# Optimization experiments

Hardware: AMD Instinct MI355X
Metric: run time of the kernel (lower is better)

The kernel has to match this reference:

```python
import jax, jax.numpy as jnp
import numpy as np

LP, LQ, B, IN, HID = 256, 256, 32, 512, 512
H = 2 * HID          # internal hidden size (hidden_size * 2)
IN2 = 2 * IN         # Up/Uq feature dim after self-concat
IN4 = 4 * IN


def setup_inputs() -> dict:
    key = jax.random.key(0)
    ks = jax.random.split(key, 12)
    def w(k, shape, fan):
        return (jax.random.normal(k, shape, jnp.float32) / np.float32(np.sqrt(fan)))
    return {
        "up": jax.random.normal(ks[0], (LP, B, IN), jnp.float32),
        "uq": jax.random.normal(ks[1], (LQ, B, IN), jnp.float32),
        "v0": jax.random.normal(ks[2], (B, H), jnp.float32),    # torch.randn v
        "Vvec": jax.random.normal(ks[3], (B, H), jnp.float32),  # torch.randn V (squeezed)
        "Wp": w(ks[4], (H, IN2), IN2),
        "Wq": w(ks[5], (H, IN2), IN2),
        "Wv": w(ks[6], (H, H), H),
        "Wg": w(ks[7], (IN4, IN4), IN4),
        "W_ih": w(ks[8], (3 * H, IN2), IN2),
        "W_hh": w(ks[9], (3 * H, H), H),
        "b_ih": w(ks[10], (3 * H,), H),
        "b_hh": w(ks[11], (3 * H,), H),
    }


def reference(up, uq, v0, Vvec, Wp, Wq, Wv, Wg, W_ih, W_hh, b_ih, b_hh):
    in2 = 2 * up.shape[2]
    # mixer indices are arange -> Up/Uq are just feature self-concats
    Up = jnp.concatenate([up, up], axis=2)   # [lp, B, in2]
    Uq = jnp.concatenate([uq, uq], axis=2)   # [lq, B, in2]
    # hoist loop-invariant projections (original recomputes Wq(Uq) each step)
    WUp = jnp.einsum('pbi,hi->pbh', Up, Wp)  # [lp, B, H]
    WUq = jnp.einsum('qbi,hi->qbh', Uq, Wq)  # [lq, B, H]

    def gru_cell(x, h):
        gi = x @ W_ih.T + b_ih
        gh = h @ W_hh.T + b_hh
        i_r, i_z, i_n = jnp.split(gi, 3, axis=1)
        h_r, h_z, h_n = jnp.split(gh, 3, axis=1)
        r = jax.nn.sigmoid(i_r + h_r)
        z = jax.nn.sigmoid(i_z + h_z)
        n = jnp.tanh(i_n + r * h_n)
        return (1.0 - z) * n + z * h

    def step(v, xs):
        up_i, wup_i = xs                                   # [B,in2], [B,H]
        x = jnp.tanh(wup_i[None] + WUq + (v @ Wv.T)[None])  # [lq, B, H]
        s = jnp.einsum('qbh,bh->bq', x, Vvec)               # [B, lq]
        a = jax.nn.softmax(s, axis=1)
        c = jnp.einsum('bq,qbd->bd', a, Uq)                 # [B, in2]
        r = jnp.concatenate([up_i, c], axis=1)              # [B, in4]
        g = jax.nn.sigmoid(r @ Wg.T)
        c_ = (g * r)[:, in2:]                               # gated context half
        v_new = gru_cell(c_, v)
        return v_new, v_new

    _, vs = jax.lax.scan(step, v0, (Up, WUp))   # vs: [lp, B, H]
    # dropout in eval mode = identity
    return vs
```

## Files before the change

### kernel.cpp

```cpp
#include <hip/hip_runtime.h>


#define NB 32
#define H 1024
#define H3 3072
#define LQn 256
#define LPn 256

__device__ __forceinline__ float fsig(float x) { return 1.0f / (1.0f + __expf(-x)); }
__device__ __forceinline__ float ftanh(float x) { return 1.0f - 2.0f / (1.0f + __expf(2.0f * x)); }

__global__ __launch_bounds__(256) void k_init(
    const float* __restrict__ v0, const float* __restrict__ Wp,
    const float* __restrict__ Wg, float* __restrict__ vbuf0,
    float* __restrict__ Wpf, float* __restrict__ Wg2f) {
  int i = blockIdx.x * 256 + threadIdx.x;
  if (i < NB * H) vbuf0[i] = v0[i];
  if (i < 1024 * 512) {
    int n = i >> 9, k = i & 511;
    Wpf[i] = Wp[(size_t)n * 1024 + k] + Wp[(size_t)n * 1024 + k + 512];
  }
  if (i < 1024 * 1024) {
    int j = i >> 10, kk = i & 1023;
    const float* wr = Wg + (size_t)(1024 + j) * 2048;
    Wg2f[i] = (kk < 512) ? (wr[kk] + wr[kk + 512]) : (wr[kk + 512] + wr[kk + 1024]);
  }
}

__global__ __launch_bounds__(256) void k_wuq(
    const float* __restrict__ A, const float* __restrict__ Wq, float* __restrict__ C) {
  __shared__ float As[16][65];
  __shared__ float Bs[16][65];
  int bm = blockIdx.x * 64, bn = blockIdx.y * 64;
  int t = threadIdx.x;
  int tx = t & 15, ty = t >> 4;
  float acc[4][4] = {};
  for (int k0 = 0; k0 < 512; k0 += 16) {
#pragma unroll
    for (int l = 0; l < 4; ++l) {
      int idx = t + l * 256;
      int row = idx >> 4, kk = idx & 15;
      As[kk][row] = A[(size_t)(bm + row) * 512 + k0 + kk];
      Bs[kk][row] = Wq[(size_t)(bn + row) * 1024 + k0 + kk] +
                    Wq[(size_t)(bn + row) * 1024 + k0 + kk + 512];
    }
    __syncthreads();
#pragma unroll
    for (int kk = 0; kk < 16; ++kk) {
      float a0[4], b0[4];
#pragma unroll
      for (int i = 0; i < 4; ++i) a0[i] = As[kk][ty * 4 + i];
#pragma unroll
      for (int j = 0; j < 4; ++j) b0[j] = Bs[kk][tx * 4 + j];
#pragma unroll
      for (int i = 0; i < 4; ++i)
#pragma unroll
        for (int j = 0; j < 4; ++j) acc[i][j] += a0[i] * b0[j];
    }
    __syncthreads();
  }
#pragma unroll
  for (int i = 0; i < 4; ++i)
#pragma unroll
    for (int j = 0; j < 4; ++j)
      C[(size_t)(bm + ty * 4 + i) * 1024 + bn + tx * 4 + j] = acc[i][j];
}

__global__ __launch_bounds__(256, 1) void k_A(
    const float* __restrict__ gi, const float* __restrict__ gh_old,
    const float* __restrict__ v_old, const float* __restrict__ up,
    const float* __restrict__ Wv, const float* __restrict__ W_hh,
    const float* __restrict__ b_hh, const float* __restrict__ Wpf,
    float* __restrict__ v_new_g, float* __restrict__ out,
    float* __restrict__ t_out, float* __restrict__ gh_new, int p) {
  int s = blockIdx.x & 63, bg = blockIdx.x >> 6;
  int b0 = bg * 8;
  int tid = threadIdx.x, lane = tid & 63, wave = tid >> 6;
  __shared__ float vnew[8][H];
  __shared__ float upb[8][512];

  if (p == 0) {
    for (int bb = 0; bb < 8; ++bb)
#pragma unroll
      for (int ii = 0; ii < 4; ++ii) {
        int h = tid + ii * 256;
        vnew[bb][h] = v_old[(size_t)(b0 + bb) * H + h];
      }
  } else {
    for (int bb = 0; bb < 8; ++bb) {
      int b = b0 + bb;
      const float* gib = gi + (size_t)b * H3;
      const float* ghb = gh_old + (size_t)b * H3;
#pragma unroll
      for (int ii = 0; ii < 4; ++ii) {
        int h = tid + ii * 256;
        float rg = fsig(gib[h] + ghb[h]);
        float z = fsig(gib[H + h] + ghb[H + h]);
        float nn = ftanh(gib[2 * H + h] + rg * ghb[2 * H + h]);
        float vo = v_old[(size_t)b * H + h];
        float vn = (1.0f - z) * nn + z * vo;
        vnew[bb][h] = vn;
        if (s == 0) {
          v_new_g[(size_t)b * H + h] = vn;
          out[((size_t)(p - 1) * NB + b) * H + h] = vn;
        }
      }
    }
  }
  bool is_t = (s < 16);
  if (is_t) {
    for (int idx = tid; idx < 8 * 512; idx += 256) {
      int bb = idx >> 9, k = idx & 511;
      upb[bb][k] = up[((size_t)p * NB + (b0 + bb)) * 512 + k];
    }
  }
  __syncthreads();

  float vreg[8][16];
#pragma unroll
  for (int bb = 0; bb < 8; ++bb)
#pragma unroll
    for (int i = 0; i < 16; ++i) vreg[bb][i] = vnew[bb][lane + i * 64];

  int n0 = s * 64 + wave * 16;
  for (int rr = 0; rr < 16; ++rr) {
    int n = n0 + rr;
    float acc[8];
#pragma unroll
    for (int bb = 0; bb < 8; ++bb) acc[bb] = 0.0f;
    if (is_t) {
      const float* wr = Wv + (size_t)n * H;
#pragma unroll
      for (int i = 0; i < 16; ++i) {
        float w = wr[lane + i * 64];
#pragma unroll
        for (int bb = 0; bb < 8; ++bb) acc[bb] = fmaf(w, vreg[bb][i], acc[bb]);
      }
      const float* wp = Wpf + (size_t)n * 512;
#pragma unroll
      for (int i = 0; i < 8; ++i) {
        float w = wp[lane + i * 64];
#pragma unroll
        for (int bb = 0; bb < 8; ++bb) acc[bb] = fmaf(w, upb[bb][lane + i * 64], acc[bb]);
      }
#pragma unroll
      for (int bb = 0; bb < 8; ++bb) {
        float a = acc[bb];
#pragma unroll
        for (int o = 32; o >= 1; o >>= 1) a += __shfl_xor(a, o, 64);
        if (lane == 0) t_out[(size_t)(b0 + bb) * H + n] = a;
      }
    } else {
      int m = n - H;
      const float* wr = W_hh + (size_t)m * H;
#pragma unroll
      for (int i = 0; i < 16; ++i) {
        float w = wr[lane + i * 64];
#pragma unroll
        for (int bb = 0; bb < 8; ++bb) acc[bb] = fmaf(w, vreg[bb][i], acc[bb]);
      }
      float bias = b_hh[m];
#pragma unroll
      for (int bb = 0; bb < 8; ++bb) {
        float a = acc[bb];
#pragma unroll
        for (int o = 32; o >= 1; o >>= 1) a += __shfl_xor(a, o, 64);
        if (lane == 0) gh_new[(size_t)(b0 + bb) * H3 + m] = a + bias;
      }
    }
  }
}

__global__ __launch_bounds__(64) void k_B(
    const float* __restrict__ t_in, const float* __restrict__ WUq,
    const float* __restrict__ Vvec, float* __restrict__ s_out) {
  int q = blockIdx.x >> 5, b = blockIdx.x & 31;
  int lane = threadIdx.x;
  const float* wq = WUq + ((size_t)q * NB + b) * H;
  const float* tb = t_in + (size_t)b * H;
  const float* vv = Vvec + (size_t)b * H;
  float a = 0.0f;
#pragma unroll
  for (int i = 0; i < 16; ++i) {
    int h = lane + i * 64;
    a += ftanh(tb[h] + wq[h]) * vv[h];
  }
#pragma unroll
  for (int o = 32; o >= 1; o >>= 1) a += __shfl_xor(a, o, 64);
  if (lane == 0) s_out[b * LQn + q] = a;
}

__global__ __launch_bounds__(256) void k_C(
    const float* __restrict__ s_in, const float* __restrict__ uq,
    const float* __restrict__ up, float* __restrict__ rhalf, int p) {
  int b = blockIdx.x;
  int tid = threadIdx.x, lane = tid & 63, wave = tid >> 6;
  __shared__ float a_s[256];
  __shared__ float red[4];
  float sv = s_in[b * LQn + tid];
  float m = sv;
#pragma unroll
  for (int o = 32; o >= 1; o >>= 1) m = fmaxf(m, __shfl_xor(m, o, 64));
  if (lane == 0) red[wave] = m;
  __syncthreads();
  float bm = fmaxf(fmaxf(red[0], red[1]), fmaxf(red[2], red[3]));
  __syncthreads();
  float e = __expf(sv - bm);
  float se = e;
#pragma unroll
  for (int o = 32; o >= 1; o >>= 1) se += __shfl_xor(se, o, 64);
  if (lane == 0) red[wave] = se;
  __syncthreads();
  float tot = red[0] + red[1] + red[2] + red[3];
  a_s[tid] = e / tot;
  __syncthreads();
  rhalf[(size_t)b * 1024 + tid] = up[((size_t)p * NB + b) * 512 + tid];
  rhalf[(size_t)b * 1024 + tid + 256] = up[((size_t)p * NB + b) * 512 + tid + 256];
  float acc0 = 0.0f, acc1 = 0.0f;
  for (int q = 0; q < LQn; ++q) {
    float a = a_s[q];
    const float* uqr = uq + ((size_t)q * NB + b) * 512;
    acc0 += a * uqr[tid];
    acc1 += a * uqr[tid + 256];
  }
  rhalf[(size_t)b * 1024 + 512 + tid] = acc0;
  rhalf[(size_t)b * 1024 + 512 + tid + 256] = acc1;
}

__global__ __launch_bounds__(256, 1) void k_D(
    const float* __restrict__ rhalf, const float* __restrict__ Wg2f,
    float* __restrict__ c_g) {
  int s = blockIdx.x & 63, bg = blockIdx.x >> 6, b0 = bg * 8;
  int tid = threadIdx.x, lane = tid & 63, wave = tid >> 6;
  float rreg[8][16];
#pragma unroll
  for (int bb = 0; bb < 8; ++bb)
#pragma unroll
    for (int i = 0; i < 16; ++i)
      rreg[bb][i] = rhalf[(size_t)(b0 + bb) * 1024 + lane + i * 64];
  int j0 = s * 16 + wave * 4;
  for (int rr = 0; rr < 4; ++rr) {
    int j = j0 + rr;
    const float* wr = Wg2f + (size_t)j * 1024;
    float acc[8];
#pragma unroll
    for (int bb = 0; bb < 8; ++bb) acc[bb] = 0.0f;
#pragma unroll
    for (int i = 0; i < 16; ++i) {
      float w = wr[lane + i * 64];
#pragma unroll
      for (int bb = 0; bb < 8; ++bb) acc[bb] = fmaf(w, rreg[bb][i], acc[bb]);
    }
#pragma unroll
    for (int bb = 0; bb < 8; ++bb) {
      float a = acc[bb];
#pragma unroll
      for (int o = 32; o >= 1; o >>= 1) a += __shfl_xor(a, o, 64);
      if (lane == 0) {
        float cv = rhalf[(size_t)(b0 + bb) * 1024 + 512 + (j & 511)];
        c_g[(size_t)(b0 + bb) * 1024 + j] = fsig(a) * cv;
      }
    }
  }
}

__global__ __launch_bounds__(256, 1) void k_E(
    const float* __restrict__ c_g, const float* __restrict__ W_ih,
    const float* __restrict__ b_ih, float* __restrict__ gi) {
  int s = blockIdx.x & 63, bg = blockIdx.x >> 6, b0 = bg * 8;
  int tid = threadIdx.x, lane = tid & 63, wave = tid >> 6;
  float creg[8][16];
#pragma unroll
  for (int bb = 0; bb < 8; ++bb)
#pragma unroll
    for (int i = 0; i < 16; ++i)
      creg[bb][i] = c_g[(size_t)(b0 + bb) * 1024 + lane + i * 64];
  int r0 = s * 48 + wave * 12;
  for (int rr = 0; rr < 12; ++rr) {
    int r = r0 + rr;
    const float* wr = W_ih + (size_t)r * 1024;
    float acc[8];
#pragma unroll
    for (int bb = 0; bb < 8; ++bb) acc[bb] = 0.0f;
#pragma unroll
    for (int i = 0; i < 16; ++i) {
      float w = wr[lane + i * 64];
#pragma unroll
      for (int bb = 0; bb < 8; ++bb) acc[bb] = fmaf(w, creg[bb][i], acc[bb]);
    }
    float bias = b_ih[r];
#pragma unroll
    for (int bb = 0; bb < 8; ++bb) {
      float a = acc[bb];
#pragma unroll
      for (int o = 32; o >= 1; o >>= 1) a += __shfl_xor(a, o, 64);
      if (lane == 0) gi[(size_t)(b0 + bb) * H3 + r] = a + bias;
    }
  }
}

__global__ __launch_bounds__(256) void k_fin(
    const float* __restrict__ gi, const float* __restrict__ gh_old,
    const float* __restrict__ v_old, float* __restrict__ out) {
  int i = blockIdx.x * 256 + threadIdx.x;
  int b = i >> 10, h = i & 1023;
  const float* gib = gi + (size_t)b * H3;
  const float* ghb = gh_old + (size_t)b * H3;
  float rg = fsig(gib[h] + ghb[h]);
  float z = fsig(gib[H + h] + ghb[H + h]);
  float nn = ftanh(gib[2 * H + h] + rg * ghb[2 * H + h]);
  float vn = (1.0f - z) * nn + z * v_old[i];
  out[(size_t)255 * NB * H + i] = vn;
}

extern "C" void kernel_launch(void* const* d_in, const int* in_sizes, int n_in,
                              void* d_out, int out_size, void* d_ws, size_t ws_size,
                              hipStream_t stream) {
  const float* up = (const float*)d_in[0];
  const float* uq = (const float*)d_in[1];
  const float* v0 = (const float*)d_in[2];
  const float* Vvec = (const float*)d_in[3];
  const float* Wp = (const float*)d_in[4];
  const float* Wq = (const float*)d_in[5];
  const float* Wv = (const float*)d_in[6];
  const float* Wg = (const float*)d_in[7];
  const float* W_ih = (const float*)d_in[8];
  const float* W_hh = (const float*)d_in[9];
  const float* b_ih = (const float*)d_in[10];
  const float* b_hh = (const float*)d_in[11];
  float* out = (float*)d_out;
  float* ws = (float*)d_ws;

  float* vbuf0 = ws;
  float* vbuf1 = ws + 32768;
  float* tbuf  = ws + 65536;
  float* gh0   = ws + 98304;
  float* gh1   = ws + 196608;
  float* sbuf  = ws + 294912;
  float* rhalf = ws + 303104;
  float* cbuf  = ws + 335872;
  float* gibuf = ws + 368640;
  float* Wpf   = ws + 466944;
  float* Wg2f  = ws + 991232;
  float* WUq   = ws + 2039808;

  k_init<<<4096, 256, 0, stream>>>(v0, Wp, Wg, vbuf0, Wpf, Wg2f);
  k_wuq<<<dim3(128, 16), 256, 0, stream>>>(uq, Wq, WUq);

  for (int p = 0; p < 256; ++p) {
    float* ghn = (p & 1) ? gh1 : gh0;
    float* gho = (p & 1) ? gh0 : gh1;
    float* vn = (p & 1) ? vbuf1 : vbuf0;
    float* vo = (p & 1) ? vbuf0 : vbuf1;
    if (p == 0) { vo = vbuf0; vn = vbuf1; }
    k_A<<<256, 256, 0, stream>>>(gibuf, gho, vo, up, Wv, W_hh, b_hh, Wpf,
                                 vn, out, tbuf, ghn, p);
    k_B<<<8192, 64, 0, stream>>>(tbuf, WUq, Vvec, sbuf);
    k_C<<<32, 256, 0, stream>>>(sbuf, uq, up, rhalf, p);
    k_D<<<256, 256, 0, stream>>>(rhalf, Wg2f, cbuf);
    k_E<<<256, 256, 0, stream>>>(cbuf, W_ih, b_ih, gibuf);
  }
  k_fin<<<128, 256, 0, stream>>>(gibuf, gh1, vbuf1, out);
}
```

Baseline: 29.62 ms.

## Replace per-step kernel launches with persistent kernel using grid barriers

Merges the five per-timestep kernels and the final kernel into one persistent kernel of 256 blocks × 512 threads. The kernel loops over all 256 steps and separates phases with a software global barrier built on atomics. The GRU update moves into the W_ih phase through shared memory, and the attention-context phase is split across 256 blocks instead of 32. This removes about 1280 launch overheads and gaps. It depends on all 256 blocks being co-resident for the spin barrier, and each barrier adds atomic latency.

```diff
diff --git a/kernel.cpp b/kernel.cpp
--- a/kernel.cpp
+++ b/kernel.cpp
@@ -2,20 +2,41 @@
 
 
 #define NB 32
-#define H 1024
-#define H3 3072
-#define LQn 256
-#define LPn 256
 
 __device__ __forceinline__ float fsig(float x) { return 1.0f / (1.0f + __expf(-x)); }
 __device__ __forceinline__ float ftanh(float x) { return 1.0f - 2.0f / (1.0f + __expf(2.0f * x)); }
 
+__device__ __forceinline__ float wred(float a) {
+#pragma unroll
+  for (int o = 32; o >= 1; o >>= 1) a += __shfl_xor(a, o, 64);
+  return a;
+}
+
+__device__ __forceinline__ void gbar(int* cnt, int* gen) {
+  __syncthreads();
+  if (threadIdx.x == 0) {
+    __threadfence();
+    int g = __hip_atomic_load(gen, __ATOMIC_RELAXED, __HIP_MEMORY_SCOPE_AGENT);
+    int a = __hip_atomic_fetch_add(cnt, 1, __ATOMIC_ACQ_REL, __HIP_MEMORY_SCOPE_AGENT);
+    if (a == 255) {
+      __hip_atomic_store(cnt, 0, __ATOMIC_RELAXED, __HIP_MEMORY_SCOPE_AGENT);
+      __hip_atomic_store(gen, g + 1, __ATOMIC_RELEASE, __HIP_MEMORY_SCOPE_AGENT);
+    } else {
+      while (__hip_atomic_load(gen, __ATOMIC_ACQUIRE, __HIP_MEMORY_SCOPE_AGENT) == g)
+        __builtin_amdgcn_s_sleep(2);
+    }
+    __threadfence();
+  }
+  __syncthreads();
+}
+
 __global__ __launch_bounds__(256) void k_init(
     const float* __restrict__ v0, const float* __restrict__ Wp,
-    const float* __restrict__ Wg, float* __restrict__ vbuf0,
-    float* __restrict__ Wpf, float* __restrict__ Wg2f) {
+    const float* __restrict__ Wg, float* __restrict__ wsbase,
+    float* __restrict__ vbuf, float* __restrict__ Wpf, float* __restrict__ Wg2f) {
   int i = blockIdx.x * 256 + threadIdx.x;
-  if (i < NB * H) vbuf0[i] = v0[i];
+  if (i < 64) ((int*)wsbase)[i] = 0;
+  if (i < NB * 1024) vbuf[i] = v0[i];
   if (i < 1024 * 512) {
     int n = i >> 9, k = i & 511;
     Wpf[i] = Wp[(size_t)n * 1024 + k] + Wp[(size_t)n * 1024 + k + 512];
@@ -66,251 +87,241 @@
       C[(size_t)(bm + ty * 4 + i) * 1024 + bn + tx * 4 + j] = acc[i][j];
 }
 
-__global__ __launch_bounds__(256, 1) void k_A(
-    const float* __restrict__ gi, const float* __restrict__ gh_old,
-    const float* __restrict__ v_old, const float* __restrict__ up,
-    const float* __restrict__ Wv, const float* __restrict__ W_hh,
-    const float* __restrict__ b_hh, const float* __restrict__ Wpf,
-    float* __restrict__ v_new_g, float* __restrict__ out,
-    float* __restrict__ t_out, float* __restrict__ gh_new, int p) {
-  int s = blockIdx.x & 63, bg = blockIdx.x >> 6;
-  int b0 = bg * 8;
+__global__ __launch_bounds__(512, 2) void k_loop(
+    const float* __restrict__ up, const float* __restrict__ uq,
+    const float* __restrict__ Vvec, const float* __restrict__ Wv,
+    const float* __restrict__ W_hh, const float* __restrict__ b_hh,
+    const float* __restrict__ W_ih, const float* __restrict__ b_ih,
+    float* __restrict__ out, float* __restrict__ ws) {
+  int* cnt = (int*)ws;
+  int* gen = ((int*)ws) + 32;
+  float* vbuf  = ws + 64;
+  float* tbuf  = ws + 32832;
+  float* ghbuf = ws + 65600;
+  float* sbuf  = ws + 163904;
+  float* chalf = ws + 172096;
+  float* cbuf  = ws + 188480;
+  float* Wpf   = ws + 221248;
+  float* Wg2f  = ws + 745536;
+  float* WUq   = ws + 1794112;
+
+  int bid = blockIdx.x;
   int tid = threadIdx.x, lane = tid & 63, wave = tid >> 6;
-  __shared__ float vnew[8][H];
-  __shared__ float upb[8][512];
-
-  if (p == 0) {
-    for (int bb = 0; bb < 8; ++bb)
-#pragma unroll
-      for (int ii = 0; ii < 4; ++ii) {
-        int h = tid + ii * 256;
-        vnew[bb][h] = v_old[(size_t)(b0 + bb) * H + h];
-      }
-  } else {
-    for (int bb = 0; bb < 8; ++bb) {
-      int b = b0 + bb;
-      const float* gib = gi + (size_t)b * H3;
-      const float* ghb = gh_old + (size_t)b * H3;
-#pragma unroll
-      for (int ii = 0; ii < 4; ++ii) {
-        int h = tid + ii * 256;
-        float rg = fsig(gib[h] + ghb[h]);
-        float z = fsig(gib[H + h] + ghb[H + h]);
-        float nn = ftanh(gib[2 * H + h] + rg * ghb[2 * H + h]);
-        float vo = v_old[(size_t)b * H + h];
+
+  __shared__ float smem[4096];
+
+  int s = bid & 63, bg = bid >> 6, b0 = bg * 8;
+  bool is_t = (s < 16);
+  int b3 = bid >> 3, i0 = (bid & 7) * 64;
+
+  for (int p = 0; p < 256; ++p) {
+    {
+      float vreg[8][16];
+#pragma unroll
+      for (int bb = 0; bb < 8; ++bb)
+#pragma unroll
+        for (int i = 0; i < 16; ++i)
+          vreg[bb][i] = vbuf[(size_t)(b0 + bb) * 1024 + lane + i * 64];
+      if (is_t) {
+        for (int idx = tid; idx < 4096; idx += 512) {
+          int bb = idx >> 9, k = idx & 511;
+          smem[idx] = up[((size_t)p * NB + b0 + bb) * 512 + k];
+        }
+      }
+      __syncthreads();
+      int n0 = s * 64 + wave * 8;
+      for (int rr = 0; rr < 8; ++rr) {
+        int n = n0 + rr;
+        float acc[8];
+#pragma unroll
+        for (int bb = 0; bb < 8; ++bb) acc[bb] = 0.0f;
+        if (is_t) {
+          const float* wr = Wv + (size_t)n * 1024;
+#pragma unroll
+          for (int i = 0; i < 16; ++i) {
+            float w = wr[lane + i * 64];
+#pragma unroll
+            for (int bb = 0; bb < 8; ++bb) acc[bb] = fmaf(w, vreg[bb][i], acc[bb]);
+          }
+          const float* wp = Wpf + (size_t)n * 512;
+#pragma unroll
+          for (int i = 0; i < 8; ++i) {
+            float w = wp[lane + i * 64];
+#pragma unroll
+            for (int bb = 0; bb < 8; ++bb)
+              acc[bb] = fmaf(w, smem[bb * 512 + lane + i * 64], acc[bb]);
+          }
+#pragma unroll
+          for (int bb = 0; bb < 8; ++bb) {
+            float a = wred(acc[bb]);
+            if (lane == 0) tbuf[(size_t)(b0 + bb) * 1024 + n] = a;
+          }
+        } else {
+          int m = n - 1024;
+          const float* wr = W_hh + (size_t)m * 1024;
+#pragma unroll
+          for (int i = 0; i < 16; ++i) {
+            float w = wr[lane + i * 64];
+#pragma unroll
+            for (int bb = 0; bb < 8; ++bb) acc[bb] = fmaf(w, vreg[bb][i], acc[bb]);
+          }
+          float bias = b_hh[m];
+#pragma unroll
+          for (int bb = 0; bb < 8; ++bb) {
+            float a = wred(acc[bb]);
+            if (lane == 0) ghbuf[(size_t)(b0 + bb) * 3072 + m] = a + bias;
+          }
+        }
+      }
+    }
+    gbar(cnt, gen);
+
+    {
+      int gw = bid * 8 + wave;
+      int b = gw & 31, q0 = (gw >> 5) * 4;
+      float treg[16], vvreg[16];
+#pragma unroll
+      for (int i = 0; i < 16; ++i) {
+        treg[i]  = tbuf[(size_t)b * 1024 + lane + i * 64];
+        vvreg[i] = Vvec[(size_t)b * 1024 + lane + i * 64];
+      }
+      for (int qq = 0; qq < 4; ++qq) {
+        int q = q0 + qq;
+        const float* wu = WUq + ((size_t)q * NB + b) * 1024;
+        float a = 0.0f;
+#pragma unroll
+        for (int i = 0; i < 16; ++i)
+          a += ftanh(treg[i] + wu[lane + i * 64]) * vvreg[i];
+        a = wred(a);
+        if (lane == 0) sbuf[b * 256 + q] = a;
+      }
+    }
+    gbar(cnt, gen);
+
+    {
+      float* a_s  = smem;
+      float* red  = smem + 256;
+      float* part = smem + 512;
+      int b = b3;
+      float sv = -1e30f;
+      if (tid < 256) sv = sbuf[b * 256 + tid];
+      float m = sv;
+#pragma unroll
+      for (int o = 32; o >= 1; o >>= 1) m = fmaxf(m, __shfl_xor(m, o, 64));
+      if (lane == 0 && wave < 4) red[wave] = m;
+      __syncthreads();
+      float bm = fmaxf(fmaxf(red[0], red[1]), fmaxf(red[2], red[3]));
+      __syncthreads();
+      float e = 0.0f;
+      if (tid < 256) e = __expf(sv - bm);
+      float se = e;
+#pragma unroll
+      for (int o = 32; o >= 1; o >>= 1) se += __shfl_xor(se, o, 64);
+      if (lane == 0 && wave < 4) red[wave] = se;
+      __syncthreads();
+      float tot = red[0] + red[1] + red[2] + red[3];
+      if (tid < 256) a_s[tid] = e / tot;
+      __syncthreads();
+      float acc = 0.0f;
+      for (int qq = 0; qq < 32; ++qq) {
+        int q = wave * 32 + qq;
+        acc += a_s[q] * uq[((size_t)q * NB + b) * 512 + i0 + lane];
+      }
+      part[wave * 64 + lane] = acc;
+      __syncthreads();
+      if (tid < 64) {
+        float c = 0.0f;
+#pragma unroll
+        for (int w = 0; w < 8; ++w) c += part[w * 64 + tid];
+        chalf[(size_t)b * 512 + i0 + tid] = c;
+      }
+    }
+    gbar(cnt, gen);
+
+    {
+      float rreg[8][16];
+#pragma unroll
+      for (int bb = 0; bb < 8; ++bb) {
+#pragma unroll
+        for (int i = 0; i < 8; ++i)
+          rreg[bb][i] = up[((size_t)p * NB + b0 + bb) * 512 + lane + i * 64];
+#pragma unroll
+        for (int i = 0; i < 8; ++i)
+          rreg[bb][8 + i] = chalf[(size_t)(b0 + bb) * 512 + lane + i * 64];
+      }
+      int j0 = s * 16 + wave * 2;
+      for (int rr = 0; rr < 2; ++rr) {
+        int j = j0 + rr;
+        const float* wr = Wg2f + (size_t)j * 1024;
+        float acc[8];
+#pragma unroll
+        for (int bb = 0; bb < 8; ++bb) acc[bb] = 0.0f;
+#pragma unroll
+        for (int i = 0; i < 16; ++i) {
+          float w = wr[lane + i * 64];
+#pragma unroll
+          for (int bb = 0; bb < 8; ++bb) acc[bb] = fmaf(w, rreg[bb][i], acc[bb]);
+        }
+#pragma unroll
+        for (int bb = 0; bb < 8; ++bb) {
+          float a = wred(acc[bb]);
+          if (lane == 0) {
+            float cv = chalf[(size_t)(b0 + bb) * 512 + (j & 511)];
+            cbuf[(size_t)(b0 + bb) * 1024 + j] = fsig(a) * cv;
+          }
+        }
+      }
+    }
+    gbar(cnt, gen);
+
+    {
+      float creg[8][16];
+#pragma unroll
+      for (int bb = 0; bb < 8; ++bb)
+#pragma unroll
+        for (int i = 0; i < 16; ++i)
+          creg[bb][i] = cbuf[(size_t)(b0 + bb) * 1024 + lane + i * 64];
+      float* gi_s = smem;
+      for (int k = 0; k < 6; ++k) {
+        int idx = wave * 6 + k;
+        int g = idx >> 4, ho = idx & 15;
+        int r = g * 1024 + s * 16 + ho;
+        const float* wr = W_ih + (size_t)r * 1024;
+        float acc[8];
+#pragma unroll
+        for (int bb = 0; bb < 8; ++bb) acc[bb] = 0.0f;
+#pragma unroll
+        for (int i = 0; i < 16; ++i) {
+          float w = wr[lane + i * 64];
+#pragma unroll
+          for (int bb = 0; bb < 8; ++bb) acc[bb] = fmaf(w, creg[bb][i], acc[bb]);
+        }
+        float bias = b_ih[r];
+#pragma unroll
+        for (int bb = 0; bb < 8; ++bb) {
+          float a = wred(acc[bb]);
+          if (lane == 0) gi_s[idx * 8 + bb] = a + bias;
+        }
+      }
+      __syncthreads();
+      if (tid < 128) {
+        int ho = tid >> 3, bb = tid & 7;
+        int h = s * 16 + ho, b = b0 + bb;
+        const float* ghb = ghbuf + (size_t)b * 3072;
+        float gir = gi_s[(0 * 16 + ho) * 8 + bb];
+        float giz = gi_s[(1 * 16 + ho) * 8 + bb];
+        float gin = gi_s[(2 * 16 + ho) * 8 + bb];
+        float rg = fsig(gir + ghb[h]);
+        float z  = fsig(giz + ghb[1024 + h]);
+        float nn = ftanh(gin + rg * ghb[2048 + h]);
+        float vo = vbuf[(size_t)b * 1024 + h];
         float vn = (1.0f - z) * nn + z * vo;
-        vnew[bb][h] = vn;
-        if (s == 0) {
-          v_new_g[(size_t)b * H + h] = vn;
-          out[((size_t)(p - 1) * NB + b) * H + h] = vn;
-        }
-      }
-    }
-  }
-  bool is_t = (s < 16);
-  if (is_t) {
-    for (int idx = tid; idx < 8 * 512; idx += 256) {
-      int bb = idx >> 9, k = idx & 511;
-      upb[bb][k] = up[((size_t)p * NB + (b0 + bb)) * 512 + k];
-    }
-  }
-  __syncthreads();
-
-  float vreg[8][16];
-#pragma unroll
-  for (int bb = 0; bb < 8; ++bb)
-#pragma unroll
-    for (int i = 0; i < 16; ++i) vreg[bb][i] = vnew[bb][lane + i * 64];
-
-  int n0 = s * 64 + wave * 16;
-  for (int rr = 0; rr < 16; ++rr) {
-    int n = n0 + rr;
-    float acc[8];
-#pragma unroll
-    for (int bb = 0; bb < 8; ++bb) acc[bb] = 0.0f;
-    if (is_t) {
-      const float* wr = Wv + (size_t)n * H;
-#pragma unroll
-      for (int i = 0; i < 16; ++i) {
-        float w = wr[lane + i * 64];
-#pragma unroll
-        for (int bb = 0; bb < 8; ++bb) acc[bb] = fmaf(w, vreg[bb][i], acc[bb]);
-      }
-      const float* wp = Wpf + (size_t)n * 512;
-#pragma unroll
-      for (int i = 0; i < 8; ++i) {
-        float w = wp[lane + i * 64];
-#pragma unroll
-        for (int bb = 0; bb < 8; ++bb) acc[bb] = fmaf(w, upb[bb][lane + i * 64], acc[bb]);
-      }
-#pragma unroll
-      for (int bb = 0; bb < 8; ++bb) {
-        float a = acc[bb];
-#pragma unroll
-        for (int o = 32; o >= 1; o >>= 1) a += __shfl_xor(a, o, 64);
-        if (lane == 0) t_out[(size_t)(b0 + bb) * H + n] = a;
-      }
-    } else {
-      int m = n - H;
-      const float* wr = W_hh + (size_t)m * H;
-#pragma unroll
-      for (int i = 0; i < 16; ++i) {
-        float w = wr[lane + i * 64];
-#pragma unroll
-        for (int bb = 0; bb < 8; ++bb) acc[bb] = fmaf(w, vreg[bb][i], acc[bb]);
-      }
-      float bias = b_hh[m];
-#pragma unroll
-      for (int bb = 0; bb < 8; ++bb) {
-        float a = acc[bb];
-#pragma unroll
-        for (int o = 32; o >= 1; o >>= 1) a += __shfl_xor(a, o, 64);
-        if (lane == 0) gh_new[(size_t)(b0 + bb) * H3 + m] = a + bias;
-      }
-    }
-  }
-}
-
-__global__ __launch_bounds__(64) void k_B(
-    const float* __restrict__ t_in, const float* __restrict__ WUq,
-    const float* __restrict__ Vvec, float* __restrict__ s_out) {
-  int q = blockIdx.x >> 5, b = blockIdx.x & 31;
-  int lane = threadIdx.x;
-  const float* wq = WUq + ((size_t)q * NB + b) * H;
-  const float* tb = t_in + (size_t)b * H;
-  const float* vv = Vvec + (size_t)b * H;
-  float a = 0.0f;
-#pragma unroll
-  for (int i = 0; i < 16; ++i) {
-    int h = lane + i * 64;
-    a += ftanh(tb[h] + wq[h]) * vv[h];
-  }
-#pragma unroll
-  for (int o = 32; o >= 1; o >>= 1) a += __shfl_xor(a, o, 64);
-  if (lane == 0) s_out[b * LQn + q] = a;
-}
-
-__global__ __launch_bounds__(256) void k_C(
-    const float* __restrict__ s_in, const float* __restrict__ uq,
-    const float* __restrict__ up, float* __restrict__ rhalf, int p) {
-  int b = blockIdx.x;
-  int tid = threadIdx.x, lane = tid & 63, wave = tid >> 6;
-  __shared__ float a_s[256];
-  __shared__ float red[4];
-  float sv = s_in[b * LQn + tid];
-  float m = sv;
-#pragma unroll
-  for (int o = 32; o >= 1; o >>= 1) m = fmaxf(m, __shfl_xor(m, o, 64));
-  if (lane == 0) red[wave] = m;
-  __syncthreads();
-  float bm = fmaxf(fmaxf(red[0], red[1]), fmaxf(red[2], red[3]));
-  __syncthreads();
-  float e = __expf(sv - bm);
-  float se = e;
-#pragma unroll
-  for (int o = 32; o >= 1; o >>= 1) se += __shfl_xor(se, o, 64);
-  if (lane == 0) red[wave] = se;
-  __syncthreads();
-  float tot = red[0] + red[1] + red[2] + red[3];
-  a_s[tid] = e / tot;
-  __syncthreads();
-  rhalf[(size_t)b * 1024 + tid] = up[((size_t)p * NB + b) * 512 + tid];
-  rhalf[(size_t)b * 1024 + tid + 256] = up[((size_t)p * NB + b) * 512 + tid + 256];
-  float acc0 = 0.0f, acc1 = 0.0f;
-  for (int q = 0; q < LQn; ++q) {
-    float a = a_s[q];
-    const float* uqr = uq + ((size_t)q * NB + b) * 512;
-    acc0 += a * uqr[tid];
-    acc1 += a * uqr[tid + 256];
-  }
-  rhalf[(size_t)b * 1024 + 512 + tid] = acc0;
-  rhalf[(size_t)b * 1024 + 512 + tid + 256] = acc1;
-}
-
-__global__ __launch_bounds__(256, 1) void k_D(
-    const float* __restrict__ rhalf, const float* __restrict__ Wg2f,
-    float* __restrict__ c_g) {
-  int s = blockIdx.x & 63, bg = blockIdx.x >> 6, b0 = bg * 8;
-  int tid = threadIdx.x, lane = tid & 63, wave = tid >> 6;
-  float rreg[8][16];
-#pragma unroll
-  for (int bb = 0; bb < 8; ++bb)
-#pragma unroll
-    for (int i = 0; i < 16; ++i)
-      rreg[bb][i] = rhalf[(size_t)(b0 + bb) * 1024 + lane + i * 64];
-  int j0 = s * 16 + wave * 4;
-  for (int rr = 0; rr < 4; ++rr) {
-    int j = j0 + rr;
-    const float* wr = Wg2f + (size_t)j * 1024;
-    float acc[8];
-#pragma unroll
-    for (int bb = 0; bb < 8; ++bb) acc[bb] = 0.0f;
-#pragma unroll
-    for (int i = 0; i < 16; ++i) {
-      float w = wr[lane + i * 64];
-#pragma unroll
-      for (int bb = 0; bb < 8; ++bb) acc[bb] = fmaf(w, rreg[bb][i], acc[bb]);
-    }
-#pragma unroll
-    for (int bb = 0; bb < 8; ++bb) {
-      float a = acc[bb];
-#pragma unroll
-      for (int o = 32; o >= 1; o >>= 1) a += __shfl_xor(a, o, 64);
-      if (lane == 0) {
-        float cv = rhalf[(size_t)(b0 + bb) * 1024 + 512 + (j & 511)];
-        c_g[(size_t)(b0 + bb) * 1024 + j] = fsig(a) * cv;
-      }
-    }
-  }
-}
-
-__global__ __launch_bounds__(256, 1) void k_E(
-    const float* __restrict__ c_g, const float* __restrict__ W_ih,
-    const float* __restrict__ b_ih, float* __restrict__ gi) {
-  int s = blockIdx.x & 63, bg = blockIdx.x >> 6, b0 = bg * 8;
-  int tid = threadIdx.x, lane = tid & 63, wave = tid >> 6;
-  float creg[8][16];
-#pragma unroll
-  for (int bb = 0; bb < 8; ++bb)
-#pragma unroll
-    for (int i = 0; i < 16; ++i)
-      creg[bb][i] = c_g[(size_t)(b0 + bb) * 1024 + lane + i * 64];
-  int r0 = s * 48 + wave * 12;
-  for (int rr = 0; rr < 12; ++rr) {
-    int r = r0 + rr;
-    const float* wr = W_ih + (size_t)r * 1024;
-    float acc[8];
-#pragma unroll
-    for (int bb = 0; bb < 8; ++bb) acc[bb] = 0.0f;
-#pragma unroll
-    for (int i = 0; i < 16; ++i) {
-      float w = wr[lane + i * 64];
-#pragma unroll
-      for (int bb = 0; bb < 8; ++bb) acc[bb] = fmaf(w, creg[bb][i], acc[bb]);
-    }
-    float bias = b_ih[r];
-#pragma unroll
-    for (int bb = 0; bb < 8; ++bb) {
-      float a = acc[bb];
-#pragma unroll
-      for (int o = 32; o >= 1; o >>= 1) a += __shfl_xor(a, o, 64);
-      if (lane == 0) gi[(size_t)(b0 + bb) * H3 + r] = a + bias;
-    }
-  }
-}
-
-__global__ __launch_bounds__(256) void k_fin(
-    const float* __restrict__ gi, const float* __restrict__ gh_old,
-    const float* __restrict__ v_old, float* __restrict__ out) {
-  int i = blockIdx.x * 256 + threadIdx.x;
-  int b = i >> 10, h = i & 1023;
-  const float* gib = gi + (size_t)b * H3;
-  const float* ghb = gh_old + (size_t)b * H3;
-  float rg = fsig(gib[h] + ghb[h]);
-  float z = fsig(gib[H + h] + ghb[H + h]);
-  float nn = ftanh(gib[2 * H + h] + rg * ghb[2 * H + h]);
-  float vn = (1.0f - z) * nn + z * v_old[i];
-  out[(size_t)255 * NB * H + i] = vn;
+        vbuf[(size_t)b * 1024 + h] = vn;
+        out[((size_t)p * NB + b) * 1024 + h] = vn;
+      }
+    }
+    gbar(cnt, gen);
+  }
 }
 
 extern "C" void kernel_launch(void* const* d_in, const int* in_sizes, int n_in,
@@ -331,34 +342,12 @@
   float* out = (float*)d_out;
   float* ws = (float*)d_ws;
 
-  float* vbuf0 = ws;
-  float* vbuf1 = ws + 32768;
-  float* tbuf  = ws + 65536;
-  float* gh0   = ws + 98304;
-  float* gh1   = ws + 196608;
-  float* sbuf  = ws + 294912;
-  float* rhalf = ws + 303104;
-  float* cbuf  = ws + 335872;
-  float* gibuf = ws + 368640;
-  float* Wpf   = ws + 466944;
-  float* Wg2f  = ws + 991232;
-  float* WUq   = ws + 2039808;
-
-  k_init<<<4096, 256, 0, stream>>>(v0, Wp, Wg, vbuf0, Wpf, Wg2f);
+  float* vbuf = ws + 64;
+  float* Wpf  = ws + 221248;
+  float* Wg2f = ws + 745536;
+  float* WUq  = ws + 1794112;
+
+  k_init<<<4096, 256, 0, stream>>>(v0, Wp, Wg, ws, vbuf, Wpf, Wg2f);
   k_wuq<<<dim3(128, 16), 256, 0, stream>>>(uq, Wq, WUq);
-
-  for (int p = 0; p < 256; ++p) {
-    float* ghn = (p & 1) ? gh1 : gh0;
-    float* gho = (p & 1) ? gh0 : gh1;
-    float* vn = (p & 1) ? vbuf1 : vbuf0;
-    float* vo = (p & 1) ? vbuf0 : vbuf1;
-    if (p == 0) { vo = vbuf0; vn = vbuf1; }
-    k_A<<<256, 256, 0, stream>>>(gibuf, gho, vo, up, Wv, W_hh, b_hh, Wpf,
-                                 vn, out, tbuf, ghn, p);
-    k_B<<<8192, 64, 0, stream>>>(tbuf, WUq, Vvec, sbuf);
-    k_C<<<32, 256, 0, stream>>>(sbuf, uq, up, rhalf, p);
-    k_D<<<256, 256, 0, stream>>>(rhalf, Wg2f, cbuf);
-    k_E<<<256, 256, 0, stream>>>(cbuf, W_ih, b_ih, gibuf);
-  }
-  k_fin<<<128, 256, 0, stream>>>(gibuf, gh1, vbuf1, out);
-}
+  k_loop<<<256, 512, 0, stream>>>(up, uq, Vvec, Wv, W_hh, b_hh, W_ih, b_ih, out, ws);
+}
```

After: 63.77 ms. 2.15x slower.
